# Optimization experiments

Hardware: AMD Instinct MI355X
Metric: run time of the kernel (lower is better)

Reference implementation:

```python
import jax, jax.numpy as jnp
import numpy as np

NUM_USERS = 100000  # n_users; embedding table has NUM_USERS+1 rows
NUM_ITEMS = 50000
D = 64
N_LAYERS = 3
N_TOTAL = NUM_USERS + 1 + NUM_ITEMS  # 150001
N_EDGES = 2_000_000
BATCH = 8192


def setup_inputs() -> dict:
    key = jax.random.key(0)
    ks = jax.random.split(key, 8)
    users = jax.random.randint(ks[0], (BATCH,), 0, NUM_USERS + 1, dtype=jnp.int32)
    items = jax.random.randint(ks[1], (BATCH,), 0, NUM_ITEMS, dtype=jnp.int32)
    labels = jax.random.uniform(ks[2], (BATCH,), dtype=jnp.float32)
    edge_row = jax.random.randint(ks[3], (N_EDGES,), 0, N_TOTAL, dtype=jnp.int32)
    edge_col = jax.random.randint(ks[4], (N_EDGES,), 0, N_TOTAL, dtype=jnp.int32)
    # mimic symmetric-normalized adjacency values ~ 1/sqrt(du*di)
    edge_val = jax.random.uniform(ks[5], (N_EDGES,), dtype=jnp.float32) / 32.0
    user_emb = jax.random.normal(ks[6], (NUM_USERS + 1, D), dtype=jnp.float32) * 0.1
    item_emb = jax.random.normal(ks[7], (NUM_ITEMS, D), dtype=jnp.float32) * 0.1
    return {"users": users, "items": items, "labels": labels,
            "edge_row": edge_row, "edge_col": edge_col, "edge_val": edge_val,
            "user_emb": user_emb, "item_emb": item_emb}


def _computer(user_emb, item_emb, edge_row, edge_col, edge_val):
    # LightGCN propagation: all_emb <- A @ all_emb, layer-wise mean pooling
    all_emb = jnp.concatenate([user_emb, item_emb], axis=0)  # [N, D]
    embs = [all_emb]
    for _ in range(N_LAYERS):
        msg = edge_val[:, None] * all_emb[edge_col]  # [E, D]
        all_emb = jax.ops.segment_sum(msg, edge_row, num_segments=N_TOTAL)
        embs.append(all_emb)
    light_out = jnp.mean(jnp.stack(embs, axis=1), axis=1)  # [N, D]
    return light_out[:NUM_USERS + 1], light_out[NUM_USERS + 1:]


def reference(users, items, labels, edge_row, edge_col, edge_val, user_emb, item_emb):
    all_users, all_items = _computer(user_emb, item_emb, edge_row, edge_col, edge_val)
    u = all_users[users]  # [B, D]
    v = all_items[items]  # [B, D]
    gamma = jnp.sum(u * v, axis=1)  # logits [B]
    y = labels.astype(gamma.dtype)
    # BCEWithLogitsLoss (mean): max(x,0) - x*y + log1p(exp(-|x|))
    loss = jnp.mean(jnp.maximum(gamma, 0) - gamma * y + jnp.log1p(jnp.exp(-jnp.abs(gamma))))
    return loss
```

## Files before the change

### kernel.cpp

```cpp
#include <hip/hip_runtime.h>
#include <hip/hip_fp16.h>

#define D 64
#define RB 512
#define RB_SHIFT 9
#define COL_BITS 18
#define COL_MASK 0x3FFFF
#define CHUNK 4096
#define FT 512

__global__ void convhist_kernel(const float* __restrict__ user_emb,
                                const float* __restrict__ item_emb,
                                __half* __restrict__ tbl,
                                int n_user_rows, int n_total,
                                const int* __restrict__ row,
                                int* __restrict__ hist, int n_edges, int nb,
                                int* __restrict__ cursor,
                                float* __restrict__ out) {
    __shared__ int h[RB];
    int blk = blockIdx.x;
    if (blk == 0) {
        if (threadIdx.x < 2) cursor[threadIdx.x] = 0;
        if (threadIdx.x == 0) out[0] = 0.0f;
    }
    for (int i = threadIdx.x; i < nb; i += FT) h[i] = 0;
    __syncthreads();
    int s = blk * CHUNK;
    int e = min(s + CHUNK, n_edges);
    for (int k = s + threadIdx.x; k < e; k += FT)
        atomicAdd(&h[row[k] >> RB_SHIFT], 1);
    __syncthreads();
    for (int i = threadIdx.x; i < nb; i += FT)
        hist[blk * nb + i] = h[i];
    size_t t = (size_t)blk * FT + threadIdx.x;
    size_t total4 = (size_t)n_total * (D / 4);
    size_t user4 = (size_t)n_user_rows * (D / 4);
    size_t stride = (size_t)gridDim.x * FT;
    for (size_t i = t; i < total4; i += stride) {
        float4 v = (i < user4) ? reinterpret_cast<const float4*>(user_emb)[i]
                               : reinterpret_cast<const float4*>(item_emb)[i - user4];
        __half2 h01 = __halves2half2(__float2half_rn(v.x), __float2half_rn(v.y));
        __half2 h23 = __halves2half2(__float2half_rn(v.z), __float2half_rn(v.w));
        uint2 o;
        o.x = *reinterpret_cast<unsigned*>(&h01);
        o.y = *reinterpret_cast<unsigned*>(&h23);
        reinterpret_cast<uint2*>(tbl)[i] = o;
    }
}

__global__ void col_alloc_kernel(int* __restrict__ hist,
                                 int* __restrict__ cstart, int* __restrict__ cend,
                                 int* __restrict__ cursor, int nb, int nblk) {
    int w = (blockIdx.x * blockDim.x + threadIdx.x) >> 6;
    int lane = threadIdx.x & 63;
    if (w >= nb) return;
    int ssum = 0;
    for (int blk = lane; blk < nblk; blk += 64)
        ssum += hist[blk * nb + w];
    for (int off = 32; off > 0; off >>= 1)
        ssum += __shfl_down(ssum, off, 64);
    int base = 0;
    if (lane == 0) base = atomicAdd(cursor, ssum);
    base = __shfl(base, 0, 64);
    int run = base;
    int total = __shfl(ssum, 0, 64);
    if (lane == 0) { cstart[w] = base; cend[w] = base + total; }
    for (int b0 = 0; b0 < nblk; b0 += 64) {
        int blk = b0 + lane;
        int v = (blk < nblk) ? hist[blk * nb + w] : 0;
        int inc = v;
#pragma unroll
        for (int off = 1; off < 64; off <<= 1) {
            int t = __shfl_up(inc, off, 64);
            if (lane >= off) inc += t;
        }
        if (blk < nblk) hist[blk * nb + w] = run + (inc - v);
        run += __shfl(inc, 63, 64);
    }
}

__global__ void fill_exact_kernel(const int* __restrict__ row, const int* __restrict__ col,
                                  const float* __restrict__ val, const int* __restrict__ hist,
                                  int2* __restrict__ stage, int n_edges, int nb) {
    __shared__ int hloc[RB];
    __shared__ int lbase[RB];
    __shared__ int gbase[RB];
    __shared__ int wsum[FT / 64];
    __shared__ int2 sdata[CHUNK];
    __shared__ int  saddr[CHUNK];
    int blk = blockIdx.x;
    int tid = threadIdx.x;
    int lane = tid & 63, wid = tid >> 6;
    for (int i = tid; i < nb; i += FT) {
        hloc[i] = 0;
        gbase[i] = hist[blk * nb + i];
    }
    __syncthreads();
    int s = blk * CHUNK;
    int e = min(s + CHUNK, n_edges);
    int cnt = e - s;
    int2 data[8];
    int bkt[8], rnk[8];
    int nloc = 0;
#pragma unroll
    for (int j = 0; j < 8; ++j) {
        int k = s + j * FT + tid;
        if (k < e) {
            int r = row[k];
            int b = r >> RB_SHIFT;
            data[nloc] = make_int2(col[k] | ((r & (RB - 1)) << COL_BITS),
                                   __float_as_int(val[k]));
            bkt[nloc] = b;
            rnk[nloc] = atomicAdd(&hloc[b], 1);
            ++nloc;
        }
    }
    __syncthreads();
    int v = (tid < nb) ? hloc[tid] : 0;
    int inc = v;
#pragma unroll
    for (int off = 1; off < 64; off <<= 1) {
        int t = __shfl_up(inc, off, 64);
        if (lane >= off) inc += t;
    }
    if (lane == 63) wsum[wid] = inc;
    __syncthreads();
    if (wid == 0) {
        int wv = (lane < FT / 64) ? wsum[lane] : 0;
        int wi = wv;
#pragma unroll
        for (int off = 1; off < FT / 64; off <<= 1) {
            int t = __shfl_up(wi, off, 64);
            if (lane >= off) wi += t;
        }
        if (lane < FT / 64) wsum[lane] = wi - wv;
    }
    __syncthreads();
    if (tid < nb) lbase[tid] = (inc - v) + wsum[wid];
    __syncthreads();
    for (int j = 0; j < nloc; ++j) {
        int b = bkt[j];
        int pos = lbase[b] + rnk[j];
        sdata[pos] = data[j];
        saddr[pos] = gbase[b] + rnk[j];
    }
    __syncthreads();
    for (int j = tid; j < cnt; j += FT)
        stage[saddr[j]] = sdata[j];
}

__global__ void bucket_pad_kernel(const int* __restrict__ cstart,
                                  const int* __restrict__ cend,
                                  const int2* __restrict__ stage,
                                  int2* __restrict__ offs,
                                  int2* __restrict__ pairs,
                                  int* __restrict__ cursor, int n_total) {
    __shared__ int sc[RB];
    __shared__ int cur[RB];
    __shared__ int wsum[RB / 64];
    __shared__ int pbase_s;
    int b = blockIdx.x;
    int tid = threadIdx.x;
    int lane = tid & 63, wid = tid >> 6;
    int s = cstart[b], e = cend[b];
    sc[tid] = 0;
    __syncthreads();
    for (int k = s + tid; k < e; k += RB)
        atomicAdd(&sc[stage[k].x >> COL_BITS], 1);
    __syncthreads();
    int cnt = sc[tid];
    int pad = (cnt + 7) & ~7;
    int inc = pad;
#pragma unroll
    for (int off = 1; off < 64; off <<= 1) {
        int t = __shfl_up(inc, off, 64);
        if (lane >= off) inc += t;
    }
    if (lane == 63) wsum[wid] = inc;
    __syncthreads();
    if (wid == 0) {
        int wv = (lane < RB / 64) ? wsum[lane] : 0;
        int wi = wv;
#pragma unroll
        for (int off = 1; off < RB / 64; off <<= 1) {
            int t = __shfl_up(wi, off, 64);
            if (lane >= off) wi += t;
        }
        if (lane < RB / 64) wsum[lane] = wi - wv;
    }
    __syncthreads();
    int incl = inc + wsum[wid];
    if (tid == RB - 1) pbase_s = atomicAdd(cursor, incl);
    __syncthreads();
    int start = pbase_s + incl - pad;
    int r = b * RB + tid;
    if (r < n_total) offs[r] = make_int2(start, start + pad);
    cur[tid] = start;
    for (int q = start + cnt; q < start + pad; ++q)
        pairs[q] = make_int2(0, 0);
    __syncthreads();
    for (int k = s + tid; k < e; k += RB) {
        int2 p = stage[k];
        int rl = p.x >> COL_BITS;
        int pos = atomicAdd(&cur[rl], 1);
        __half hw = __float2half_rn(__int_as_float(p.y));
        unsigned hb = (unsigned)*reinterpret_cast<unsigned short*>(&hw);
        pairs[pos] = make_int2(p.x & COL_MASK, (int)(hb | (hb << 16)));
    }
}

__device__ __forceinline__ void step4(const int2* __restrict__ pairs, int k,
                                      const uint4* __restrict__ s4, int sub,
                                      __half2 acc[4]) {
    uint4 qa = reinterpret_cast<const uint4*>(pairs + k)[0];
    uint4 qb = reinterpret_cast<const uint4*>(pairs + k)[1];
    uint4 r0 = s4[(size_t)qa.x * 8 + sub];
    uint4 r1 = s4[(size_t)qa.z * 8 + sub];
    uint4 r2 = s4[(size_t)qb.x * 8 + sub];
    uint4 r3 = s4[(size_t)qb.z * 8 + sub];
    __half2 w0 = *reinterpret_cast<__half2*>(&qa.y);
    __half2 w1 = *reinterpret_cast<__half2*>(&qa.w);
    __half2 w2 = *reinterpret_cast<__half2*>(&qb.y);
    __half2 w3 = *reinterpret_cast<__half2*>(&qb.w);
    const __half2* h0 = reinterpret_cast<const __half2*>(&r0);
    const __half2* h1 = reinterpret_cast<const __half2*>(&r1);
    const __half2* h2 = reinterpret_cast<const __half2*>(&r2);
    const __half2* h3 = reinterpret_cast<const __half2*>(&r3);
#pragma unroll
    for (int i = 0; i < 4; ++i) {
        acc[i] = __hfma2(h0[i], w0, acc[i]);
        acc[i] = __hfma2(h1[i], w1, acc[i]);
        acc[i] = __hfma2(h2[i], w2, acc[i]);
        acc[i] = __hfma2(h3[i], w3, acc[i]);
    }
}

__global__ void spmm_gather_kernel(const int2* __restrict__ offs,
                                   const int2* __restrict__ pairs,
                                   const __half* __restrict__ src,
                                   __half* __restrict__ dst, int n_total) {
    int t = blockIdx.x * blockDim.x + threadIdx.x;
    int r = t >> 3;
    int sub = t & 7;
    if (r >= n_total) return;
    int2 oo = offs[r];
    const uint4* s4 = reinterpret_cast<const uint4*>(src);
    __half2 acc[4];
    acc[0] = __float2half2_rn(0.f);
    acc[1] = acc[0]; acc[2] = acc[0]; acc[3] = acc[0];
    for (int k = oo.x; k < oo.y; k += 8) {
        step4(pairs, k, s4, sub, acc);
        step4(pairs, k + 4, s4, sub, acc);
    }
    reinterpret_cast<uint4*>(dst + (size_t)r * D)[sub] =
        *reinterpret_cast<uint4*>(acc);
}

__global__ void batch_loss_kernel(const int* __restrict__ users,
                                  const int* __restrict__ items,
                                  const int2* __restrict__ offs,
                                  const int2* __restrict__ pairs,
                                  const float* __restrict__ user_emb,
                                  const float* __restrict__ item_emb,
                                  const __half* __restrict__ buf0,
                                  const __half* __restrict__ buf1,
                                  const float* __restrict__ labels,
                                  float* __restrict__ out,
                                  int batch, int n_user_rows) {
    int t = blockIdx.x * blockDim.x + threadIdx.x;
    int b = t >> 3;
    int sub = t & 7;
    const uint4* s4 = reinterpret_cast<const uint4*>(buf1);
    float lb = 0.0f;
    if (b < batch) {
        float uf[8], vf[8];
        int u = users[b];
        int it = items[b];
        {
            float4 e0 = reinterpret_cast<const float4*>(user_emb + (size_t)u * D)[sub * 2];
            float4 e1 = reinterpret_cast<const float4*>(user_emb + (size_t)u * D)[sub * 2 + 1];
            uf[0] = e0.x; uf[1] = e0.y; uf[2] = e0.z; uf[3] = e0.w;
            uf[4] = e1.x; uf[5] = e1.y; uf[6] = e1.z; uf[7] = e1.w;
            float4 f0 = reinterpret_cast<const float4*>(item_emb + (size_t)it * D)[sub * 2];
            float4 f1 = reinterpret_cast<const float4*>(item_emb + (size_t)it * D)[sub * 2 + 1];
            vf[0] = f0.x; vf[1] = f0.y; vf[2] = f0.z; vf[3] = f0.w;
            vf[4] = f1.x; vf[5] = f1.y; vf[6] = f1.z; vf[7] = f1.w;
        }
        int urow = u;
        int vrow = n_user_rows + it;
        {
            uint4 x0 = reinterpret_cast<const uint4*>(buf0 + (size_t)urow * D)[sub];
            uint4 x1 = reinterpret_cast<const uint4*>(buf1 + (size_t)urow * D)[sub];
            uint4 y0 = reinterpret_cast<const uint4*>(buf0 + (size_t)vrow * D)[sub];
            uint4 y1 = reinterpret_cast<const uint4*>(buf1 + (size_t)vrow * D)[sub];
            const __half2* p0 = reinterpret_cast<const __half2*>(&x0);
            const __half2* p1 = reinterpret_cast<const __half2*>(&x1);
            const __half2* q0 = reinterpret_cast<const __half2*>(&y0);
            const __half2* q1 = reinterpret_cast<const __half2*>(&y1);
#pragma unroll
            for (int i = 0; i < 4; ++i) {
                float2 f0 = __half22float2(p0[i]);
                float2 f1 = __half22float2(p1[i]);
                uf[2 * i] += f0.x + f1.x;
                uf[2 * i + 1] += f0.y + f1.y;
                float2 g0 = __half22float2(q0[i]);
                float2 g1 = __half22float2(q1[i]);
                vf[2 * i] += g0.x + g1.x;
                vf[2 * i + 1] += g0.y + g1.y;
            }
        }
        __half2 z = __float2half2_rn(0.f);
        __half2 au[4] = {z, z, z, z};
        __half2 av[4] = {z, z, z, z};
        int2 ou = offs[urow];
        int2 ov = offs[vrow];
        for (int k = ou.x; k < ou.y; k += 8) {
            step4(pairs, k, s4, sub, au);
            step4(pairs, k + 4, s4, sub, au);
        }
        for (int k = ov.x; k < ov.y; k += 8) {
            step4(pairs, k, s4, sub, av);
            step4(pairs, k + 4, s4, sub, av);
        }
        float partial = 0.0f;
#pragma unroll
        for (int i = 0; i < 4; ++i) {
            float2 fa = __half22float2(au[i]);
            float2 fc = __half22float2(av[i]);
            partial += (uf[2 * i] + fa.x) * (vf[2 * i] + fc.x);
            partial += (uf[2 * i + 1] + fa.y) * (vf[2 * i + 1] + fc.y);
        }
        partial += __shfl_xor(partial, 1, 64);
        partial += __shfl_xor(partial, 2, 64);
        partial += __shfl_xor(partial, 4, 64);
        if (sub == 0) {
            float g = partial * (1.0f / 16.0f);
            float y = labels[b];
            lb = fmaxf(g, 0.0f) - g * y + log1pf(expf(-fabsf(g)));
        }
    }
    lb += __shfl_xor(lb, 8, 64);
    lb += __shfl_xor(lb, 16, 64);
    lb += __shfl_xor(lb, 32, 64);
    __shared__ float sd[4];
    int wid = threadIdx.x >> 6;
    if ((threadIdx.x & 63) == 0) sd[wid] = lb;
    __syncthreads();
    if (threadIdx.x == 0)
        atomicAdd(out, (sd[0] + sd[1] + sd[2] + sd[3]) / (float)batch);
}

extern "C" void kernel_launch(void* const* d_in, const int* in_sizes, int n_in,
                              void* d_out, int out_size, void* d_ws, size_t ws_size,
                              hipStream_t stream) {
    const int* users = (const int*)d_in[0];
    const int* items = (const int*)d_in[1];
    const float* labels = (const float*)d_in[2];
    const int* edge_row = (const int*)d_in[3];
    const int* edge_col = (const int*)d_in[4];
    const float* edge_val = (const float*)d_in[5];
    const float* user_emb = (const float*)d_in[6];
    const float* item_emb = (const float*)d_in[7];

    const int batch = in_sizes[0];
    const int n_edges = in_sizes[3];
    const int n_user_rows = in_sizes[6] / D;
    const int n_item_rows = in_sizes[7] / D;
    const int n_total = n_user_rows + n_item_rows;
    const int nb = (n_total + RB - 1) / RB;
    const int nblk = (n_edges + CHUNK - 1) / CHUNK;
    const int L = nb * nblk;
    const int max_pairs = n_edges + 7 * nb * RB;

    auto align256 = [](size_t x) { return (x + 255) & ~(size_t)255; };
    const size_t tblb_bytes = align256((size_t)n_total * D * 2);
    const size_t offs_bytes = align256((size_t)n_total * sizeof(int2));
    const size_t pairs_bytes = align256((size_t)max_pairs * sizeof(int2));
    const size_t hist_bytes = align256((size_t)L * sizeof(int));
    const size_t cse_bytes = align256((size_t)nb * sizeof(int));

    char* ws = (char*)d_ws;
    __half* tbl  = (__half*)ws;                  ws += tblb_bytes;
    __half* buf0 = (__half*)ws;                  ws += tblb_bytes;
    __half* buf1 = (__half*)ws;                  ws += tblb_bytes;
    int2*  offs   = (int2*)ws;                   ws += offs_bytes;
    int2*  pairs  = (int2*)ws;                   ws += pairs_bytes;
    int*   cursor = (int*)ws;                    ws += 256;
    int2*  stage  = (int2*)buf0;
    char* sb = (char*)buf1;
    int* hist   = (int*)sb;                      sb += hist_bytes;
    int* cstart = (int*)sb;                      sb += cse_bytes;
    int* cend   = (int*)sb;                      sb += cse_bytes;

    convhist_kernel<<<nblk, FT, 0, stream>>>(user_emb, item_emb, tbl,
                                             n_user_rows, n_total,
                                             edge_row, hist, n_edges, nb,
                                             cursor, (float*)d_out);

    const int wave_blocks = (nb + 3) / 4;
    col_alloc_kernel<<<wave_blocks, 256, 0, stream>>>(hist, cstart, cend,
                                                      &cursor[0], nb, nblk);
    fill_exact_kernel<<<nblk, FT, 0, stream>>>(edge_row, edge_col, edge_val,
                                               hist, stage, n_edges, nb);
    bucket_pad_kernel<<<nb, RB, 0, stream>>>(cstart, cend, stage, offs, pairs,
                                             &cursor[1], n_total);

    const int spmm_blocks = (int)(((size_t)n_total * 8 + 255) / 256);
    spmm_gather_kernel<<<spmm_blocks, 256, 0, stream>>>(offs, pairs, tbl, buf0, n_total);
    spmm_gather_kernel<<<spmm_blocks, 256, 0, stream>>>(offs, pairs, buf0, buf1, n_total);

    const int bl_blocks = (batch * 8 + 255) / 256;
    batch_loss_kernel<<<bl_blocks, 256, 0, stream>>>(users, items, offs, pairs,
                                                     user_emb, item_emb, buf0, buf1,
                                                     labels, (float*)d_out,
                                                     batch, n_user_rows);
}
```

Measured before the change: 158.9 us.

## Store embeddings and edge weights in FP8 with packed 4-byte edge entries

Converts the propagated embedding tables from fp16 to fp8 (E4M3 via the cvt_pk_fp8 builtins) and packs each edge into one 32-bit word holding an 18-bit column and an 8-bit fp8 weight. Accumulation is moved to fp32. This halves gather bytes per neighbor row and halves the edge-list traffic in the SpMM and loss kernels. The cost is a large precision loss: fp8 embeddings and weights with small magnitudes (around 0.1 and below 1/32) may lose significant accuracy or underflow, which could break tolerance. The stage and hist buffers no longer alias the embedding buffers, so the workspace grows.

```diff
diff --git a/kernel.cpp b/kernel.cpp
--- a/kernel.cpp
+++ b/kernel.cpp
@@ -9,9 +9,11 @@
 #define CHUNK 4096
 #define FT 512
 
+typedef float floatx2 __attribute__((ext_vector_type(2)));
+
 __global__ void convhist_kernel(const float* __restrict__ user_emb,
                                 const float* __restrict__ item_emb,
-                                __half* __restrict__ tbl,
+                                unsigned char* __restrict__ tbl,
                                 int n_user_rows, int n_total,
                                 const int* __restrict__ row,
                                 int* __restrict__ hist, int n_edges, int nb,
@@ -39,12 +41,9 @@
     for (size_t i = t; i < total4; i += stride) {
         float4 v = (i < user4) ? reinterpret_cast<const float4*>(user_emb)[i]
                                : reinterpret_cast<const float4*>(item_emb)[i - user4];
-        __half2 h01 = __halves2half2(__float2half_rn(v.x), __float2half_rn(v.y));
-        __half2 h23 = __halves2half2(__float2half_rn(v.z), __float2half_rn(v.w));
-        uint2 o;
-        o.x = *reinterpret_cast<unsigned*>(&h01);
-        o.y = *reinterpret_cast<unsigned*>(&h23);
-        reinterpret_cast<uint2*>(tbl)[i] = o;
+        int o = __builtin_amdgcn_cvt_pk_fp8_f32(v.x, v.y, 0, false);
+        o = __builtin_amdgcn_cvt_pk_fp8_f32(v.z, v.w, o, true);
+        reinterpret_cast<unsigned*>(tbl)[i] = (unsigned)o;
     }
 }
 
@@ -153,7 +152,7 @@
                                   const int* __restrict__ cend,
                                   const int2* __restrict__ stage,
                                   int2* __restrict__ offs,
-                                  int2* __restrict__ pairs,
+                                  unsigned* __restrict__ pairs,
                                   int* __restrict__ cursor, int n_total) {
     __shared__ int sc[RB];
     __shared__ int cur[RB];
@@ -197,80 +196,89 @@
     if (r < n_total) offs[r] = make_int2(start, start + pad);
     cur[tid] = start;
     for (int q = start + cnt; q < start + pad; ++q)
-        pairs[q] = make_int2(0, 0);
+        pairs[q] = 0u;
     __syncthreads();
     for (int k = s + tid; k < e; k += RB) {
         int2 p = stage[k];
         int rl = p.x >> COL_BITS;
         int pos = atomicAdd(&cur[rl], 1);
-        __half hw = __float2half_rn(__int_as_float(p.y));
-        unsigned hb = (unsigned)*reinterpret_cast<unsigned short*>(&hw);
-        pairs[pos] = make_int2(p.x & COL_MASK, (int)(hb | (hb << 16)));
-    }
-}
-
-__device__ __forceinline__ void step4(const int2* __restrict__ pairs, int k,
-                                      const uint4* __restrict__ s4, int sub,
-                                      __half2 acc[4]) {
-    uint4 qa = reinterpret_cast<const uint4*>(pairs + k)[0];
-    uint4 qb = reinterpret_cast<const uint4*>(pairs + k)[1];
-    uint4 r0 = s4[(size_t)qa.x * 8 + sub];
-    uint4 r1 = s4[(size_t)qa.z * 8 + sub];
-    uint4 r2 = s4[(size_t)qb.x * 8 + sub];
-    uint4 r3 = s4[(size_t)qb.z * 8 + sub];
-    __half2 w0 = *reinterpret_cast<__half2*>(&qa.y);
-    __half2 w1 = *reinterpret_cast<__half2*>(&qa.w);
-    __half2 w2 = *reinterpret_cast<__half2*>(&qb.y);
-    __half2 w3 = *reinterpret_cast<__half2*>(&qb.w);
-    const __half2* h0 = reinterpret_cast<const __half2*>(&r0);
-    const __half2* h1 = reinterpret_cast<const __half2*>(&r1);
-    const __half2* h2 = reinterpret_cast<const __half2*>(&r2);
-    const __half2* h3 = reinterpret_cast<const __half2*>(&r3);
-#pragma unroll
-    for (int i = 0; i < 4; ++i) {
-        acc[i] = __hfma2(h0[i], w0, acc[i]);
-        acc[i] = __hfma2(h1[i], w1, acc[i]);
-        acc[i] = __hfma2(h2[i], w2, acc[i]);
-        acc[i] = __hfma2(h3[i], w3, acc[i]);
-    }
+        float w = __int_as_float(p.y);
+        int pk = __builtin_amdgcn_cvt_pk_fp8_f32(w, 0.0f, 0, false);
+        pairs[pos] = (unsigned)(p.x & COL_MASK) | ((unsigned)(pk & 0xFF) << 24);
+    }
+}
+
+__device__ __forceinline__ void fma8(uint2 raw, float w, float a[8]) {
+    floatx2 f0 = __builtin_amdgcn_cvt_pk_f32_fp8((int)raw.x, false);
+    floatx2 f1 = __builtin_amdgcn_cvt_pk_f32_fp8((int)raw.x, true);
+    floatx2 f2 = __builtin_amdgcn_cvt_pk_f32_fp8((int)raw.y, false);
+    floatx2 f3 = __builtin_amdgcn_cvt_pk_f32_fp8((int)raw.y, true);
+    a[0] += w * f0[0]; a[1] += w * f0[1];
+    a[2] += w * f1[0]; a[3] += w * f1[1];
+    a[4] += w * f2[0]; a[5] += w * f2[1];
+    a[6] += w * f3[0]; a[7] += w * f3[1];
+}
+
+__device__ __forceinline__ void gather8(const unsigned* __restrict__ pairs, int k,
+                                        const uint2* __restrict__ s2, int sub,
+                                        float a[8]) {
+    uint4 qa = *reinterpret_cast<const uint4*>(pairs + k);
+    uint4 qb = *reinterpret_cast<const uint4*>(pairs + k + 4);
+    uint2 r0 = s2[(size_t)(qa.x & COL_MASK) * 8 + sub];
+    uint2 r1 = s2[(size_t)(qa.y & COL_MASK) * 8 + sub];
+    uint2 r2 = s2[(size_t)(qa.z & COL_MASK) * 8 + sub];
+    uint2 r3 = s2[(size_t)(qa.w & COL_MASK) * 8 + sub];
+    uint2 r4 = s2[(size_t)(qb.x & COL_MASK) * 8 + sub];
+    uint2 r5 = s2[(size_t)(qb.y & COL_MASK) * 8 + sub];
+    uint2 r6 = s2[(size_t)(qb.z & COL_MASK) * 8 + sub];
+    uint2 r7 = s2[(size_t)(qb.w & COL_MASK) * 8 + sub];
+    fma8(r0, __builtin_amdgcn_cvt_f32_fp8((int)qa.x, 3), a);
+    fma8(r1, __builtin_amdgcn_cvt_f32_fp8((int)qa.y, 3), a);
+    fma8(r2, __builtin_amdgcn_cvt_f32_fp8((int)qa.z, 3), a);
+    fma8(r3, __builtin_amdgcn_cvt_f32_fp8((int)qa.w, 3), a);
+    fma8(r4, __builtin_amdgcn_cvt_f32_fp8((int)qb.x, 3), a);
+    fma8(r5, __builtin_amdgcn_cvt_f32_fp8((int)qb.y, 3), a);
+    fma8(r6, __builtin_amdgcn_cvt_f32_fp8((int)qb.z, 3), a);
+    fma8(r7, __builtin_amdgcn_cvt_f32_fp8((int)qb.w, 3), a);
 }
 
 __global__ void spmm_gather_kernel(const int2* __restrict__ offs,
-                                   const int2* __restrict__ pairs,
-                                   const __half* __restrict__ src,
-                                   __half* __restrict__ dst, int n_total) {
+                                   const unsigned* __restrict__ pairs,
+                                   const unsigned char* __restrict__ src,
+                                   unsigned char* __restrict__ dst, int n_total) {
     int t = blockIdx.x * blockDim.x + threadIdx.x;
     int r = t >> 3;
     int sub = t & 7;
     if (r >= n_total) return;
     int2 oo = offs[r];
-    const uint4* s4 = reinterpret_cast<const uint4*>(src);
-    __half2 acc[4];
-    acc[0] = __float2half2_rn(0.f);
-    acc[1] = acc[0]; acc[2] = acc[0]; acc[3] = acc[0];
-    for (int k = oo.x; k < oo.y; k += 8) {
-        step4(pairs, k, s4, sub, acc);
-        step4(pairs, k + 4, s4, sub, acc);
-    }
-    reinterpret_cast<uint4*>(dst + (size_t)r * D)[sub] =
-        *reinterpret_cast<uint4*>(acc);
+    const uint2* s2 = reinterpret_cast<const uint2*>(src);
+    float a[8] = {0.f, 0.f, 0.f, 0.f, 0.f, 0.f, 0.f, 0.f};
+    for (int k = oo.x; k < oo.y; k += 8)
+        gather8(pairs, k, s2, sub, a);
+    int ox = __builtin_amdgcn_cvt_pk_fp8_f32(a[0], a[1], 0, false);
+    ox = __builtin_amdgcn_cvt_pk_fp8_f32(a[2], a[3], ox, true);
+    int oy = __builtin_amdgcn_cvt_pk_fp8_f32(a[4], a[5], 0, false);
+    oy = __builtin_amdgcn_cvt_pk_fp8_f32(a[6], a[7], oy, true);
+    uint2 o = make_uint2((unsigned)ox, (unsigned)oy);
+    reinterpret_cast<uint2*>(dst)[(size_t)r * 8 + sub] = o;
 }
 
 __global__ void batch_loss_kernel(const int* __restrict__ users,
                                   const int* __restrict__ items,
                                   const int2* __restrict__ offs,
-                                  const int2* __restrict__ pairs,
+                                  const unsigned* __restrict__ pairs,
                                   const float* __restrict__ user_emb,
                                   const float* __restrict__ item_emb,
-                                  const __half* __restrict__ buf0,
-                                  const __half* __restrict__ buf1,
+                                  const unsigned char* __restrict__ buf0,
+                                  const unsigned char* __restrict__ buf1,
                                   const float* __restrict__ labels,
                                   float* __restrict__ out,
                                   int batch, int n_user_rows) {
     int t = blockIdx.x * blockDim.x + threadIdx.x;
     int b = t >> 3;
     int sub = t & 7;
-    const uint4* s4 = reinterpret_cast<const uint4*>(buf1);
+    const uint2* s2 = reinterpret_cast<const uint2*>(buf1);
+    const uint2* s0 = reinterpret_cast<const uint2*>(buf0);
     float lb = 0.0f;
     if (b < batch) {
         float uf[8], vf[8];
@@ -288,48 +296,20 @@
         }
         int urow = u;
         int vrow = n_user_rows + it;
-        {
-            uint4 x0 = reinterpret_cast<const uint4*>(buf0 + (size_t)urow * D)[sub];
-            uint4 x1 = reinterpret_cast<const uint4*>(buf1 + (size_t)urow * D)[sub];
-            uint4 y0 = reinterpret_cast<const uint4*>(buf0 + (size_t)vrow * D)[sub];
-            uint4 y1 = reinterpret_cast<const uint4*>(buf1 + (size_t)vrow * D)[sub];
-            const __half2* p0 = reinterpret_cast<const __half2*>(&x0);
-            const __half2* p1 = reinterpret_cast<const __half2*>(&x1);
-            const __half2* q0 = reinterpret_cast<const __half2*>(&y0);
-            const __half2* q1 = reinterpret_cast<const __half2*>(&y1);
-#pragma unroll
-            for (int i = 0; i < 4; ++i) {
-                float2 f0 = __half22float2(p0[i]);
-                float2 f1 = __half22float2(p1[i]);
-                uf[2 * i] += f0.x + f1.x;
-                uf[2 * i + 1] += f0.y + f1.y;
-                float2 g0 = __half22float2(q0[i]);
-                float2 g1 = __half22float2(q1[i]);
-                vf[2 * i] += g0.x + g1.x;
-                vf[2 * i + 1] += g0.y + g1.y;
-            }
-        }
-        __half2 z = __float2half2_rn(0.f);
-        __half2 au[4] = {z, z, z, z};
-        __half2 av[4] = {z, z, z, z};
+        fma8(s0[(size_t)urow * 8 + sub], 1.0f, uf);
+        fma8(s2[(size_t)urow * 8 + sub], 1.0f, uf);
+        fma8(s0[(size_t)vrow * 8 + sub], 1.0f, vf);
+        fma8(s2[(size_t)vrow * 8 + sub], 1.0f, vf);
+        float au[8] = {0.f, 0.f, 0.f, 0.f, 0.f, 0.f, 0.f, 0.f};
+        float av[8] = {0.f, 0.f, 0.f, 0.f, 0.f, 0.f, 0.f, 0.f};
         int2 ou = offs[urow];
         int2 ov = offs[vrow];
-        for (int k = ou.x; k < ou.y; k += 8) {
-            step4(pairs, k, s4, sub, au);
-            step4(pairs, k + 4, s4, sub, au);
-        }
-        for (int k = ov.x; k < ov.y; k += 8) {
-            step4(pairs, k, s4, sub, av);
-            step4(pairs, k + 4, s4, sub, av);
-        }
+        for (int k = ou.x; k < ou.y; k += 8) gather8(pairs, k, s2, sub, au);
+        for (int k = ov.x; k < ov.y; k += 8) gather8(pairs, k, s2, sub, av);
         float partial = 0.0f;
 #pragma unroll
-        for (int i = 0; i < 4; ++i) {
-            float2 fa = __half22float2(au[i]);
-            float2 fc = __half22float2(av[i]);
-            partial += (uf[2 * i] + fa.x) * (vf[2 * i] + fc.x);
-            partial += (uf[2 * i + 1] + fa.y) * (vf[2 * i + 1] + fc.y);
-        }
+        for (int i = 0; i < 8; ++i)
+            partial += (uf[i] + au[i]) * (vf[i] + av[i]);
         partial += __shfl_xor(partial, 1, 64);
         partial += __shfl_xor(partial, 2, 64);
         partial += __shfl_xor(partial, 4, 64);
@@ -373,24 +353,24 @@
     const int max_pairs = n_edges + 7 * nb * RB;
 
     auto align256 = [](size_t x) { return (x + 255) & ~(size_t)255; };
-    const size_t tblb_bytes = align256((size_t)n_total * D * 2);
+    const size_t tblb_bytes = align256((size_t)n_total * D);
     const size_t offs_bytes = align256((size_t)n_total * sizeof(int2));
-    const size_t pairs_bytes = align256((size_t)max_pairs * sizeof(int2));
+    const size_t pairs_bytes = align256((size_t)max_pairs * sizeof(unsigned));
+    const size_t stage_bytes = align256((size_t)n_edges * sizeof(int2));
     const size_t hist_bytes = align256((size_t)L * sizeof(int));
     const size_t cse_bytes = align256((size_t)nb * sizeof(int));
 
     char* ws = (char*)d_ws;
-    __half* tbl  = (__half*)ws;                  ws += tblb_bytes;
-    __half* buf0 = (__half*)ws;                  ws += tblb_bytes;
-    __half* buf1 = (__half*)ws;                  ws += tblb_bytes;
+    unsigned char* tbl  = (unsigned char*)ws;    ws += tblb_bytes;
+    unsigned char* buf0 = (unsigned char*)ws;    ws += tblb_bytes;
+    unsigned char* buf1 = (unsigned char*)ws;    ws += tblb_bytes;
     int2*  offs   = (int2*)ws;                   ws += offs_bytes;
-    int2*  pairs  = (int2*)ws;                   ws += pairs_bytes;
+    unsigned* pairs = (unsigned*)ws;             ws += pairs_bytes;
+    int2*  stage  = (int2*)ws;                   ws += stage_bytes;
+    int*   hist   = (int*)ws;                    ws += hist_bytes;
+    int*   cstart = (int*)ws;                    ws += cse_bytes;
+    int*   cend   = (int*)ws;                    ws += cse_bytes;
     int*   cursor = (int*)ws;                    ws += 256;
-    int2*  stage  = (int2*)buf0;
-    char* sb = (char*)buf1;
-    int* hist   = (int*)sb;                      sb += hist_bytes;
-    int* cstart = (int*)sb;                      sb += cse_bytes;
-    int* cend   = (int*)sb;                      sb += cse_bytes;
 
     convhist_kernel<<<nblk, FT, 0, stream>>>(user_emb, item_emb, tbl,
                                              n_user_rows, n_total,
```

New measurement: 136.2 us. -14.3%, faster.
